# Performance work log

Measured on AMD Instinct MI355X. Metric: run time of the kernel, lower is better.

Reference implementation:

```python
import jax, jax.numpy as jnp
import numpy as np

B, S, DIM, HID, E, SE, K = 4, 2048, 1024, 1280, 8, 2, 2

def setup_inputs() -> dict:
    key = jax.random.key(0)
    ks = jax.random.split(key, 8)
    std = 0.02
    return {
        "x": jax.random.normal(ks[0], (B, S, DIM), jnp.float32),
        "expert_emb": jax.random.normal(ks[1], (E, DIM), jnp.float32),
        "gate_bias": jnp.zeros((E,), jnp.float32),
        "w1": jax.random.normal(ks[2], (E, HID, DIM), jnp.float32) * std,
        "w2": jax.random.normal(ks[3], (E, DIM, HID), jnp.float32) * std,
        "w3": jax.random.normal(ks[4], (E, HID, DIM), jnp.float32) * std,
        "sw1": jax.random.normal(ks[5], (SE, HID, DIM), jnp.float32) * std,
        "sw2": jax.random.normal(ks[6], (SE, DIM, HID), jnp.float32) * std,
        "sw3": jax.random.normal(ks[7], (SE, HID, DIM), jnp.float32) * std,
    }

def reference(x, expert_emb, gate_bias, w1, w2, w3, sw1, sw2, sw3):
    b, s, d = x.shape
    xt = x.reshape(-1, d)  # (T, D), T = B*S
    n_shared = sw1.shape[0]
    n_exp = w1.shape[0]
    k = K
    # shared experts: SwiGLU FFN, averaged over shared experts
    hs = jax.nn.silu(jnp.einsum('td,ehd->eth', xt, sw1)) * jnp.einsum('td,ehd->eth', xt, sw3)
    shared = jnp.einsum('eth,edh->td', hs, sw2) / n_shared  # mean over shared experts
    # gate: sigmoid scores + bias, top-k, normalized weights
    scores = jax.nn.sigmoid(xt @ expert_emb.T) + gate_bias  # (T, E)
    top_vals, top_idx = jax.lax.top_k(scores, k)            # (T, K)
    w = top_vals / jnp.sum(top_vals, axis=-1, keepdims=True)
    # per-token combine weight for each expert (0 if not routed)
    combine = jnp.sum((top_idx[..., None] == jnp.arange(n_exp)) * w[..., None], axis=1)  # (T, E)
    # routed experts: dense per-expert FFN, combined with routing weights
    hr = jax.nn.silu(jnp.einsum('td,ehd->eth', xt, w1)) * jnp.einsum('td,ehd->eth', xt, w3)
    out_e = jnp.einsum('eth,edh->etd', hr, w2)
    routed = jnp.einsum('etd,te->td', out_e, combine)
    out = (shared + routed).reshape(b, s, d)
    aux_loss = jnp.float32(0.0)  # eval mode: aux loss not computed
    routing_entropy = -jnp.sum(w * jnp.log(w), axis=-1).mean()
    return (out, aux_loss, routing_entropy)
```

## Files before the change

kernel.cpp:

```cpp
#include <hip/hip_runtime.h>
#include <math.h>

#define TOK 8192
#define DIMN 1024
#define HID 1280
#define NEXP 8
#define NSH 2
#define NSLOT 10
#define RCAP 17408
#define RCAPG (RCAP + 256)
#define G1_NT (DIMN / 64)
#define NGATE (TOK / 4)

typedef short s16x8 __attribute__((ext_vector_type(8)));
typedef float f32x4 __attribute__((ext_vector_type(4)));

__device__ __forceinline__ unsigned short f2bf(float f) {
  unsigned u = __float_as_uint(f);
  u += 0x7fffu + ((u >> 16) & 1u);
  return (unsigned short)(u >> 16);
}
__device__ __forceinline__ float bf2f(unsigned short u) {
  return __uint_as_float((unsigned)u << 16);
}

__device__ __forceinline__ void gl_lds16(const void* g, void* l) {
  typedef __attribute__((address_space(1))) const unsigned int guint;
  typedef __attribute__((address_space(3))) unsigned int luint;
  __builtin_amdgcn_global_load_lds((guint*)g, (luint*)l, 16, 0, 0);
}

__global__ __launch_bounds__(256) void k_zero(int* __restrict__ glist,
                                              int* __restrict__ cnt, int* __restrict__ cnt2) {
  int i = blockIdx.x * 256 + threadIdx.x;
  if (i < RCAPG) glist[i] = 0;
  if (i < NEXP) { cnt[i] = 0; cnt2[i] = 0; }
}

__global__ __launch_bounds__(256) void k_cvt_x(const float* __restrict__ x,
                                               unsigned short* __restrict__ xb) {
  int i = blockIdx.x * 256 + threadIdx.x;
  float4 v = ((const float4*)x)[i];
  ushort4 o;
  o.x = f2bf(v.x); o.y = f2bf(v.y); o.z = f2bf(v.z); o.w = f2bf(v.w);
  ((ushort4*)xb)[i] = o;
}

__global__ __launch_bounds__(256) void k_cvt_w(const float* __restrict__ w1, const float* __restrict__ w3,
                                               const float* __restrict__ sw1, const float* __restrict__ sw3,
                                               const float* __restrict__ w2, const float* __restrict__ sw2,
                                               unsigned short* __restrict__ w13b,
                                               unsigned short* __restrict__ w2b) {
  const int r = blockIdx.x;
  const int s = blockIdx.y;
  if (r < 2560) {
    const int which = (r >> 4) & 1;
    const int srow = ((r >> 5) << 4) + (r & 15);
    const float* src;
    if (s < NSH) src = (which ? sw3 : sw1) + ((size_t)s * HID + srow) * DIMN;
    else         src = (which ? w3 : w1) + ((size_t)(s - NSH) * HID + srow) * DIMN;
    unsigned short* dst = w13b + ((size_t)s * 2560 + r) * DIMN;
    int c = threadIdx.x * 4;
    float4 v = *(const float4*)(src + c);
    ushort4 o;
    o.x = f2bf(v.x); o.y = f2bf(v.y); o.z = f2bf(v.z); o.w = f2bf(v.w);
    *(ushort4*)(dst + c) = o;
  } else {
    const int d = r - 2560;
    const float* src = (s < NSH) ? sw2 + ((size_t)s * DIMN + d) * HID
                                 : w2 + ((size_t)(s - NSH) * DIMN + d) * HID;
    unsigned short* dst = w2b + ((size_t)s * DIMN + d) * HID;
    for (int c = threadIdx.x * 4; c < HID; c += 1024) {
      float4 v = *(const float4*)(src + c);
      ushort4 o;
      o.x = f2bf(v.x); o.y = f2bf(v.y); o.z = f2bf(v.z); o.w = f2bf(v.w);
      *(ushort4*)(dst + c) = o;
    }
  }
}

__global__ __launch_bounds__(256) void k_gate(const float* __restrict__ x, const float* __restrict__ emb,
                                              const float* __restrict__ bias, int* __restrict__ tidx,
                                              float* __restrict__ tw, float* __restrict__ entp) {
  const int lane = threadIdx.x & 63;
  const int wv = threadIdx.x >> 6;
  const int t = blockIdx.x * 4 + wv;
  const float* xr = x + (size_t)t * DIMN;
  float acc[NEXP];
#pragma unroll
  for (int e = 0; e < NEXP; ++e) acc[e] = 0.0f;
  for (int i = 0; i < DIMN / 64; ++i) {
    float xv = xr[lane + 64 * i];
#pragma unroll
    for (int e = 0; e < NEXP; ++e)
      acc[e] = fmaf(xv, emb[e * DIMN + lane + 64 * i], acc[e]);
  }
#pragma unroll
  for (int e = 0; e < NEXP; ++e) {
#pragma unroll
    for (int off = 32; off > 0; off >>= 1) acc[e] += __shfl_xor(acc[e], off);
  }
  __shared__ float ebuf[4];
  if (lane == 0) {
    float s[NEXP];
#pragma unroll
    for (int e = 0; e < NEXP; ++e) s[e] = 1.0f / (1.0f + expf(-acc[e])) + bias[e];
    int i0 = 0;
    for (int e = 1; e < NEXP; ++e) if (s[e] > s[i0]) i0 = e;
    int i1 = -1;
    for (int e = 0; e < NEXP; ++e) {
      if (e == i0) continue;
      if (i1 < 0 || s[e] > s[i1]) i1 = e;
    }
    float v0 = s[i0], v1 = s[i1];
    float inv = 1.0f / (v0 + v1);
    float w0 = v0 * inv, w1 = v1 * inv;
    tidx[2 * t] = i0; tidx[2 * t + 1] = i1;
    tw[2 * t] = w0; tw[2 * t + 1] = w1;
    ebuf[wv] = -(w0 * logf(w0) + w1 * logf(w1));
  }
  __syncthreads();
  if (threadIdx.x == 0) entp[blockIdx.x] = ebuf[0] + ebuf[1] + ebuf[2] + ebuf[3];
}

__global__ __launch_bounds__(256) void k_count(const int* __restrict__ tidx, int* __restrict__ cnt) {
  __shared__ int hist[NEXP];
  const int tid = threadIdx.x;
  if (tid < NEXP) hist[tid] = 0;
  __syncthreads();
  const int t = blockIdx.x * 256 + tid;
  atomicAdd(&hist[tidx[2 * t]], 1);
  atomicAdd(&hist[tidx[2 * t + 1]], 1);
  __syncthreads();
  if (tid < NEXP) atomicAdd(&cnt[tid], hist[tid]);
}

__global__ __launch_bounds__(256) void k_offsets(const int* __restrict__ cnt, int* __restrict__ roff,
                                                 int* __restrict__ cpad, const float* __restrict__ entp,
                                                 float* __restrict__ out_tail) {
  __shared__ float red[256];
  float s = 0.f;
  for (int i = threadIdx.x; i < NGATE; i += 256) s += entp[i];
  red[threadIdx.x] = s;
  __syncthreads();
  for (int st = 128; st > 0; st >>= 1) {
    if (threadIdx.x < st) red[threadIdx.x] += red[threadIdx.x + st];
    __syncthreads();
  }
  if (threadIdx.x == 0) {
    int off = 0;
    for (int e = 0; e < NEXP; ++e) {
      roff[e] = off;
      int cp = (cnt[e] + 127) & ~127;
      cpad[e] = cp;
      off += cp;
    }
    out_tail[0] = 0.f;
    out_tail[1] = red[0] / (float)TOK;
  }
}

__global__ __launch_bounds__(256) void k_scatter(const int* __restrict__ tidx,
                                                 const int* __restrict__ roff, int* __restrict__ cnt2,
                                                 int* __restrict__ glist, int* __restrict__ pos) {
  __shared__ int hist[NEXP], base[NEXP], cur[NEXP];
  const int tid = threadIdx.x;
  if (tid < NEXP) { hist[tid] = 0; cur[tid] = 0; }
  __syncthreads();
  const int t = blockIdx.x * 256 + tid;
  const int e0 = tidx[2 * t], e1 = tidx[2 * t + 1];
  atomicAdd(&hist[e0], 1);
  atomicAdd(&hist[e1], 1);
  __syncthreads();
  if (tid < NEXP) base[tid] = atomicAdd(&cnt2[tid], hist[tid]);
  __syncthreads();
  int p0 = atomicAdd(&cur[e0], 1);
  int g0 = roff[e0] + base[e0] + p0;
  glist[g0] = t; pos[2 * t] = g0;
  int p1 = atomicAdd(&cur[e1], 1);
  int g1 = roff[e1] + base[e1] + p1;
  glist[g1] = t; pos[2 * t + 1] = g1;
}

__global__ __launch_bounds__(512, 2) void k_gemm1_8ph(const unsigned short* __restrict__ xb,
                                                      const unsigned short* __restrict__ w13b,
                                                      unsigned short* __restrict__ h,
                                                      const int* __restrict__ glist,
                                                      const int* __restrict__ roff,
                                                      const int* __restrict__ cpad) {
  extern __shared__ __align__(16) char smem[];
  const int slot = blockIdx.z, yb = blockIdx.y, bx = blockIdx.x;
  const int tid = threadIdx.x;
  const int w = tid >> 6, lane = tid & 63;
  int hrow0, rowlim;
  int tokq[4];
  const int trbase = w * 8 + (lane >> 3);
  if (slot < NSH) {
    hrow0 = slot * TOK + yb * 256;
    rowlim = 256;
#pragma unroll
    for (int q = 0; q < 4; ++q) tokq[q] = yb * 256 + q * 64 + trbase;
  } else {
    const int e = slot - NSH;
    const int cp = cpad[e];
    if (yb * 256 >= cp) return;
    const int base = roff[e];
    hrow0 = 2 * TOK + base + yb * 256;
    rowlim = cp - yb * 256; if (rowlim > 256) rowlim = 256;
#pragma unroll
    for (int q = 0; q < 4; ++q) tokq[q] = glist[base + yb * 256 + q * 64 + trbase];
  }
  const int srcoff = ((lane & 7) * 16) ^ (((lane >> 4) & 1) << 4) ^ (((lane >> 5) & 1) << 5) ^ ((w & 1) << 6);
  const char* aptr[4];
#pragma unroll
  for (int q = 0; q < 4; ++q) aptr[q] = (const char*)xb + (size_t)tokq[q] * 2048 + srcoff;
  const char* w13s = (const char*)w13b + (size_t)slot * 2560 * 2048;
  const int crow0 = (w >> 2) * 64 + (w & 3) * 8 + (lane >> 3);
  const char* bptr[2];
#pragma unroll
  for (int nq = 0; nq < 2; ++nq)
    bptr[nq] = w13s + (size_t)(bx * 256 + crow0 + nq * 32) * 2048 + srcoff;
  const int dA = (w * 8) * 128;
  const int dB = 32768 + (((w >> 2) * 64 + (w & 3) * 8) * 128);

#define STA(BB, MH, TT) do {                               \
    char* _d = smem + (BB) + dA + (MH) * 8192;             \
    gl_lds16(aptr[MH] + (TT) * 128, _d);                   \
    gl_lds16(aptr[(MH) + 2] + (TT) * 128, _d + 16384);     \
  } while (0)
#define STB(BB, NQ, TT) do {                               \
    char* _d = smem + (BB) + dB + (NQ) * 4096;             \
    gl_lds16(bptr[NQ] + (TT) * 128, _d);                   \
    gl_lds16(bptr[NQ] + 262144 + (TT) * 128, _d + 16384);  \
  } while (0)

  const int lr = lane & 15, lq = lane >> 4;
  const int kswz = (((lr >> 1) & 1) << 4) | (((lr >> 2) & 1) << 5) | (((lr >> 3) & 1) << 6);
  const int wm = w >> 2, wn = w & 3;
  const int aoffb = (wm * 128 + lr) * 128 + lq * 16;
  const int boffb = 32768 + (wn * 64 + lr) * 128 + lq * 16;

#define RD_A(BB, MH) do {                                                                            \
    _Pragma("unroll")                                                                                \
    for (int mf = 0; mf < 4; ++mf)                                                                   \
      _Pragma("unroll")                                                                              \
      for (int ks = 0; ks < 2; ++ks)                                                                 \
        areg[mf][ks] = *(const s16x8*)(smem + (((BB) + aoffb + (MH) * 8192 + mf * 2048 + ks * 64) ^ kswz)); \
  } while (0)
#define RD_B(BB, NQ, RG) do {                                                                        \
    _Pragma("unroll")                                                                                \
    for (int nf = 0; nf < 2; ++nf)                                                                   \
      _Pragma("unroll")                                                                              \
      for (int ks = 0; ks < 2; ++ks)                                                                 \
        RG[nf][ks] = *(const s16x8*)(smem + (((BB) + boffb + (NQ) * 4096 + nf * 2048 + ks * 64) ^ kswz)); \
  } while (0)
#define MFMA16(MH, RG, NQ) do {                                                                      \
    __builtin_amdgcn_s_setprio(1);                                                                   \
    _Pragma("unroll")                                                                                \
    for (int mf = 0; mf < 4; ++mf)                                                                   \
      _Pragma("unroll")                                                                              \
      for (int nf = 0; nf < 2; ++nf)                                                                 \
        _Pragma("unroll")                                                                            \
        for (int ks = 0; ks < 2; ++ks)                                                               \
          acc[(MH) * 4 + mf][(NQ) * 2 + nf] = __builtin_amdgcn_mfma_f32_16x16x32_bf16(               \
              areg[mf][ks], RG[nf][ks], acc[(MH) * 4 + mf][(NQ) * 2 + nf], 0, 0, 0);                 \
    __builtin_amdgcn_s_setprio(0);                                                                   \
  } while (0)
#define VMW(N) asm volatile("s_waitcnt vmcnt(" #N ")" ::: "memory")
#define BARR() __builtin_amdgcn_s_barrier()
#define LGKM0() asm volatile("s_waitcnt lgkmcnt(0)" ::: "memory")

  STA(0, 0, 0); STB(0, 0, 0); STA(0, 1, 0); STB(0, 1, 0);
  STA(65536, 0, 1); STB(65536, 0, 1);
  VMW(8);
  BARR();

  f32x4 acc[8][4] = {};
  for (int j = 0; j < G1_NT; ++j) {
    const int bufb = (j & 1) << 16;
    const int bufo = bufb ^ 65536;
    const int t1 = (j + 1 < G1_NT) ? j + 1 : G1_NT - 1;
    const int t2 = (j + 2 < G1_NT) ? j + 2 : G1_NT - 1;
    s16x8 areg[4][2];
    s16x8 breg0[2][2], breg1[2][2];
    RD_A(bufb, 0);
    RD_B(bufb, 0, breg0);
    STA(bufo, 1, t1);
    VMW(6);
    BARR(); LGKM0();
    MFMA16(0, breg0, 0);
    BARR();
    RD_B(bufb, 1, breg1);
    STB(bufo, 1, t1);
    BARR(); LGKM0();
    MFMA16(0, breg1, 1);
    BARR();
    RD_A(bufb, 1);
    STA(bufb, 0, t2);
    BARR(); LGKM0();
    MFMA16(1, breg1, 1);
    BARR();
    STB(bufb, 0, t2);
    VMW(8);
    BARR();
    MFMA16(1, breg0, 0);
    BARR();
  }
#undef STA
#undef STB

  asm volatile("s_waitcnt vmcnt(0)" ::: "memory");
#pragma unroll
  for (int m = 0; m < 8; ++m) {
    const int lrow0 = wm * 128 + (m >> 2) * 64 + (m & 3) * 16 + lq * 4;
#pragma unroll
    for (int p = 0; p < 2; ++p) {
      f32x4 a1 = acc[m][2 * p];
      f32x4 a3 = acc[m][2 * p + 1];
      const int hc = (bx * 8 + wn * 2 + p) * 16 + lr;
#pragma unroll
      for (int r = 0; r < 4; ++r) {
        const int lrow = lrow0 + r;
        if (lrow < rowlim) {
          float u = a1[r];
          float hv = (u / (1.f + __expf(-u))) * a3[r];
          h[(size_t)(hrow0 + lrow) * HID + hc] = f2bf(hv);
        }
      }
    }
  }
#undef RD_A
#undef RD_B
#undef MFMA16
#undef VMW
#undef BARR
#undef LGKM0
}

__global__ __launch_bounds__(512, 2) void k_gemm2g(const unsigned short* __restrict__ h,
                                                   const unsigned short* __restrict__ w2b,
                                                   const int* __restrict__ roff,
                                                   const int* __restrict__ cpad,
                                                   float* __restrict__ out,
                                                   unsigned short* __restrict__ ro) {
  extern __shared__ __align__(16) char smem[];
  const int grp = blockIdx.z, bx = blockIdx.x, yb = blockIdx.y;
  const int tid = threadIdx.x;
  const int w = tid >> 6, lane = tid & 63;
  const int trbase = w * 8 + (lane >> 3);
  int nt, rowlim, base = 0;
  size_t arow0, arow1;
  if (grp == 0) {
    if (yb * 256 >= TOK) return;
    nt = 40; rowlim = 256;
    arow0 = (size_t)(yb * 256);
    arow1 = (size_t)(TOK + yb * 256);
  } else {
    const int e = grp - 1;
    const int cp = cpad[e];
    if (yb * 256 >= cp) return;
    base = roff[e];
    nt = 20;
    rowlim = cp - yb * 256; if (rowlim > 256) rowlim = 256;
    arow0 = (size_t)(2 * TOK + base + yb * 256);
    arow1 = arow0;
  }
  const int srcoff = ((lane & 7) * 16) ^ (((lane >> 4) & 1) << 4) ^ (((lane >> 5) & 1) << 5) ^ ((w & 1) << 6);
  const char* aptr0[4];
  const char* aptr1[4];
#pragma unroll
  for (int q = 0; q < 4; ++q) {
    int rq = q * 64 + trbase;
    if (grp != 0 && rq >= rowlim) rq = 0;
    aptr0[q] = (const char*)h + (arow0 + rq) * 2560 + srcoff;
    aptr1[q] = (const char*)h + (arow1 + rq) * 2560 + srcoff;
  }
  const int crow0 = (w >> 2) * 64 + (w & 3) * 8 + (lane >> 3);
  const char* bptr0[2];
  const char* bptr1[2];
#pragma unroll
  for (int nq = 0; nq < 2; ++nq) {
    const int bn = bx * 256 + crow0 + nq * 32;
    if (grp == 0) {
      bptr0[nq] = (const char*)w2b + (size_t)bn * 2560 + srcoff;
      bptr1[nq] = (const char*)w2b + (size_t)(1024 + bn) * 2560 + srcoff;
    } else {
      bptr0[nq] = (const char*)w2b + (size_t)((NSH + grp - 1) * 1024 + bn) * 2560 + srcoff;
      bptr1[nq] = bptr0[nq];
    }
  }
  const int dA = (w * 8) * 128;
  const int dB = 32768 + (((w >> 2) * 64 + (w & 3) * 8) * 128);

#define ASRC(Q, TT) ((TT) < 20 ? aptr0[Q] + (TT) * 128 : aptr1[Q] + ((TT) - 20) * 128)
#define BSRC(NQ, TT) ((TT) < 20 ? bptr0[NQ] + (TT) * 128 : bptr1[NQ] + ((TT) - 20) * 128)
#define STA(BB, MH, TT) do {                               \
    char* _d = smem + (BB) + dA + (MH) * 8192;             \
    gl_lds16(ASRC(MH, TT), _d);                            \
    gl_lds16(ASRC((MH) + 2, TT), _d + 16384);              \
  } while (0)
#define STB(BB, NQ, TT) do {                               \
    char* _d = smem + (BB) + dB + (NQ) * 4096;             \
    gl_lds16(BSRC(NQ, TT), _d);                            \
    gl_lds16(BSRC(NQ, TT) + (size_t)128 * 2560, _d + 16384); \
  } while (0)

  const int lr = lane & 15, lq = lane >> 4;
  const int kswz = (((lr >> 1) & 1) << 4) | (((lr >> 2) & 1) << 5) | (((lr >> 3) & 1) << 6);
  const int wm = w >> 2, wn = w & 3;
  const int aoffb = (wm * 128 + lr) * 128 + lq * 16;
  const int boffb = 32768 + (wn * 64 + lr) * 128 + lq * 16;

#define RD_A(BB, MH) do {                                                                            \
    _Pragma("unroll")                                                                                \
    for (int mf = 0; mf < 4; ++mf)                                                                   \
      _Pragma("unroll")                                                                              \
      for (int ks = 0; ks < 2; ++ks)                                                                 \
        areg[mf][ks] = *(const s16x8*)(smem + (((BB) + aoffb + (MH) * 8192 + mf * 2048 + ks * 64) ^ kswz)); \
  } while (0)
#define RD_B(BB, NQ, RG) do {                                                                        \
    _Pragma("unroll")                                                                                \
    for (int nf = 0; nf < 2; ++nf)                                                                   \
      _Pragma("unroll")                                                                              \
      for (int ks = 0; ks < 2; ++ks)                                                                 \
        RG[nf][ks] = *(const s16x8*)(smem + (((BB) + boffb + (NQ) * 4096 + nf * 2048 + ks * 64) ^ kswz)); \
  } while (0)
#define MFMA16(MH, RG, NQ) do {                                                                      \
    __builtin_amdgcn_s_setprio(1);                                                                   \
    _Pragma("unroll")                                                                                \
    for (int mf = 0; mf < 4; ++mf)                                                                   \
      _Pragma("unroll")                                                                              \
      for (int nf = 0; nf < 2; ++nf)                                                                 \
        _Pragma("unroll")                                                                            \
        for (int ks = 0; ks < 2; ++ks)                                                               \
          acc[(MH) * 4 + mf][(NQ) * 2 + nf] = __builtin_amdgcn_mfma_f32_16x16x32_bf16(               \
              areg[mf][ks], RG[nf][ks], acc[(MH) * 4 + mf][(NQ) * 2 + nf], 0, 0, 0);                 \
    __builtin_amdgcn_s_setprio(0);                                                                   \
  } while (0)
#define VMW(N) asm volatile("s_waitcnt vmcnt(" #N ")" ::: "memory")
#define BARR() __builtin_amdgcn_s_barrier()
#define LGKM0() asm volatile("s_waitcnt lgkmcnt(0)" ::: "memory")

  STA(0, 0, 0); STB(0, 0, 0); STA(0, 1, 0); STB(0, 1, 0);
  STA(65536, 0, 1); STB(65536, 0, 1);
  VMW(8);
  BARR();

  f32x4 acc[8][4] = {};
  for (int j = 0; j < nt; ++j) {
    const int bufb = (j & 1) << 16;
    const int bufo = bufb ^ 65536;
    const int t1 = (j + 1 < nt) ? j + 1 : nt - 1;
    const int t2 = (j + 2 < nt) ? j + 2 : nt - 1;
    s16x8 areg[4][2];
    s16x8 breg0[2][2], breg1[2][2];
    RD_A(bufb, 0);
    RD_B(bufb, 0, breg0);
    STA(bufo, 1, t1);
    VMW(6);
    BARR(); LGKM0();
    MFMA16(0, breg0, 0);
    BARR();
    RD_B(bufb, 1, breg1);
    STB(bufo, 1, t1);
    BARR(); LGKM0();
    MFMA16(0, breg1, 1);
    BARR();
    RD_A(bufb, 1);
    STA(bufb, 0, t2);
    BARR(); LGKM0();
    MFMA16(1, breg1, 1);
    BARR();
    STB(bufb, 0, t2);
    VMW(8);
    BARR();
    MFMA16(1, breg0, 0);
    BARR();
  }
#undef STA
#undef STB
#undef ASRC
#undef BSRC

  asm volatile("s_waitcnt vmcnt(0)" ::: "memory");
  if (grp == 0) {
#pragma unroll
    for (int m = 0; m < 8; ++m) {
      const int lrow0 = wm * 128 + (m >> 2) * 64 + (m & 3) * 16 + lq * 4;
#pragma unroll
      for (int nf = 0; nf < 4; ++nf) {
        const int col = bx * 256 + wn * 64 + nf * 16 + lr;
#pragma unroll
        for (int r = 0; r < 4; ++r)
          out[(size_t)(yb * 256 + lrow0 + r) * DIMN + col] = 0.5f * acc[m][nf][r];
      }
    }
  } else {
#pragma unroll
    for (int m = 0; m < 8; ++m) {
      const int lrow0 = wm * 128 + (m >> 2) * 64 + (m & 3) * 16 + lq * 4;
#pragma unroll
      for (int r = 0; r < 4; ++r) {
        const int lrow = lrow0 + r;
        if (lrow < rowlim) {
          const size_t g = (size_t)(base + yb * 256 + lrow);
#pragma unroll
          for (int nf = 0; nf < 4; ++nf) {
            const int col = bx * 256 + wn * 64 + nf * 16 + lr;
            ro[g * DIMN + col] = f2bf(acc[m][nf][r]);
          }
        }
      }
    }
  }
#undef RD_A
#undef RD_B
#undef MFMA16
#undef VMW
#undef BARR
#undef LGKM0
}

__global__ __launch_bounds__(256) void k_combine(const unsigned short* __restrict__ ro,
                                                 const int* __restrict__ pos,
                                                 const float* __restrict__ tw,
                                                 float* __restrict__ out) {
  const int t = blockIdx.x;
  const int g0 = pos[2 * t], g1 = pos[2 * t + 1];
  const float w0 = tw[2 * t], w1 = tw[2 * t + 1];
  const int c = threadIdx.x * 4;
  ushort4 r0 = *(const ushort4*)(ro + (size_t)g0 * DIMN + c);
  ushort4 r1 = *(const ushort4*)(ro + (size_t)g1 * DIMN + c);
  float4 o = *(float4*)(out + (size_t)t * DIMN + c);
  o.x += w0 * bf2f(r0.x) + w1 * bf2f(r1.x);
  o.y += w0 * bf2f(r0.y) + w1 * bf2f(r1.y);
  o.z += w0 * bf2f(r0.z) + w1 * bf2f(r1.z);
  o.w += w0 * bf2f(r0.w) + w1 * bf2f(r1.w);
  *(float4*)(out + (size_t)t * DIMN + c) = o;
}

static const size_t OFF_XB    = 0;
static const size_t OFF_W13   = OFF_XB + (size_t)TOK * DIMN * 2;
static const size_t OFF_W2    = OFF_W13 + (size_t)NSLOT * 2560 * DIMN * 2;
static const size_t OFF_H     = OFF_W2 + (size_t)NSLOT * DIMN * HID * 2;
static const size_t OFF_RO    = OFF_W13;
static const size_t OFF_GLIST = OFF_H + (size_t)(2 * TOK + RCAP) * HID * 2;
static const size_t OFF_POS   = OFF_GLIST + (size_t)RCAPG * 4;
static const size_t OFF_TIDX  = OFF_POS + (size_t)TOK * 2 * 4;
static const size_t OFF_TW    = OFF_TIDX + (size_t)TOK * 2 * 4;
static const size_t OFF_ENTP  = OFF_TW + (size_t)TOK * 2 * 4;
static const size_t OFF_CNT   = OFF_ENTP + (size_t)NGATE * 4;
static const size_t OFF_CNT2  = OFF_CNT + 32;
static const size_t OFF_ROFF  = OFF_CNT2 + 32;
static const size_t OFF_CPAD  = OFF_ROFF + 32;

extern "C" void kernel_launch(void* const* d_in, const int* in_sizes, int n_in,
                              void* d_out, int out_size, void* d_ws, size_t ws_size,
                              hipStream_t stream) {
  const float* x    = (const float*)d_in[0];
  const float* emb  = (const float*)d_in[1];
  const float* bias = (const float*)d_in[2];
  const float* w1   = (const float*)d_in[3];
  const float* w2   = (const float*)d_in[4];
  const float* w3   = (const float*)d_in[5];
  const float* sw1  = (const float*)d_in[6];
  const float* sw2  = (const float*)d_in[7];
  const float* sw3  = (const float*)d_in[8];
  float* out = (float*)d_out;
  char* ws = (char*)d_ws;
  unsigned short* xb   = (unsigned short*)(ws + OFF_XB);
  unsigned short* w13b = (unsigned short*)(ws + OFF_W13);
  unsigned short* w2b  = (unsigned short*)(ws + OFF_W2);
  unsigned short* h    = (unsigned short*)(ws + OFF_H);
  unsigned short* ro   = (unsigned short*)(ws + OFF_RO);
  int*   glist = (int*)(ws + OFF_GLIST);
  int*   pos   = (int*)(ws + OFF_POS);
  int*   tidx  = (int*)(ws + OFF_TIDX);
  float* tw    = (float*)(ws + OFF_TW);
  float* entp  = (float*)(ws + OFF_ENTP);
  int*   cnt   = (int*)(ws + OFF_CNT);
  int*   cnt2  = (int*)(ws + OFF_CNT2);
  int*   roff  = (int*)(ws + OFF_ROFF);
  int*   cpad  = (int*)(ws + OFF_CPAD);

  hipFuncSetAttribute((const void*)k_gemm1_8ph, hipFuncAttributeMaxDynamicSharedMemorySize, 131072);
  hipFuncSetAttribute((const void*)k_gemm2g, hipFuncAttributeMaxDynamicSharedMemorySize, 131072);

  k_zero<<<(RCAPG + 255) / 256, 256, 0, stream>>>(glist, cnt, cnt2);
  k_cvt_x<<<(TOK * DIMN / 4) / 256, 256, 0, stream>>>(x, xb);
  k_cvt_w<<<dim3(2560 + DIMN, NSLOT), 256, 0, stream>>>(w1, w3, sw1, sw3, w2, sw2, w13b, w2b);
  k_gate<<<NGATE, 256, 0, stream>>>(x, emb, bias, tidx, tw, entp);
  k_count<<<TOK / 256, 256, 0, stream>>>(tidx, cnt);
  k_offsets<<<1, 256, 0, stream>>>(cnt, roff, cpad, entp, out + (size_t)TOK * DIMN);
  k_scatter<<<TOK / 256, 256, 0, stream>>>(tidx, roff, cnt2, glist, pos);
  k_gemm1_8ph<<<dim3(10, TOK / 256, NSLOT), 512, 131072, stream>>>(xb, w13b, h, glist, roff, cpad);
  k_gemm2g<<<dim3(DIMN / 256, TOK / 256, 1 + NEXP), 512, 131072, stream>>>(h, w2b, roff, cpad, out, ro);
  k_combine<<<TOK, 256, 0, stream>>>(ro, pos, tw, out);
}
```

Measured before the change: 427.2 us.

## Fuse x bf16 conversion into gate and software-pipeline gemm1 LDS reads with MFMA

Removes the separate x-to-bf16 conversion kernel and writes the bf16 copy inside the gate kernel, which already reads x, saving one full pass over the activations and one launch. In gemm1, LDS fragment loads are double-buffered into separate A register sets and issued ahead of the MFMAs that use them. The explicit lgkmcnt waits are replaced by scheduling barriers so that LDS reads overlap with matrix math. The extra register arrays raise register pressure in a kernel launched with a 512-thread, two-blocks-per-unit bound. The gate kernel now does narrow 2-byte strided stores, which may coalesce poorly.

```diff
diff --git a/kernel.cpp b/kernel.cpp
--- a/kernel.cpp
+++ b/kernel.cpp
@@ -35,15 +35,6 @@
   int i = blockIdx.x * 256 + threadIdx.x;
   if (i < RCAPG) glist[i] = 0;
   if (i < NEXP) { cnt[i] = 0; cnt2[i] = 0; }
-}
-
-__global__ __launch_bounds__(256) void k_cvt_x(const float* __restrict__ x,
-                                               unsigned short* __restrict__ xb) {
-  int i = blockIdx.x * 256 + threadIdx.x;
-  float4 v = ((const float4*)x)[i];
-  ushort4 o;
-  o.x = f2bf(v.x); o.y = f2bf(v.y); o.z = f2bf(v.z); o.w = f2bf(v.w);
-  ((ushort4*)xb)[i] = o;
 }
 
 __global__ __launch_bounds__(256) void k_cvt_w(const float* __restrict__ w1, const float* __restrict__ w3,
@@ -80,17 +71,21 @@
 }
 
 __global__ __launch_bounds__(256) void k_gate(const float* __restrict__ x, const float* __restrict__ emb,
-                                              const float* __restrict__ bias, int* __restrict__ tidx,
+                                              const float* __restrict__ bias,
+                                              unsigned short* __restrict__ xb,
+                                              int* __restrict__ tidx,
                                               float* __restrict__ tw, float* __restrict__ entp) {
   const int lane = threadIdx.x & 63;
   const int wv = threadIdx.x >> 6;
   const int t = blockIdx.x * 4 + wv;
   const float* xr = x + (size_t)t * DIMN;
+  unsigned short* xbr = xb + (size_t)t * DIMN;
   float acc[NEXP];
 #pragma unroll
   for (int e = 0; e < NEXP; ++e) acc[e] = 0.0f;
   for (int i = 0; i < DIMN / 64; ++i) {
     float xv = xr[lane + 64 * i];
+    xbr[lane + 64 * i] = f2bf(xv);
 #pragma unroll
     for (int e = 0; e < NEXP; ++e)
       acc[e] = fmaf(xv, emb[e * DIMN + lane + 64 * i], acc[e]);
@@ -240,12 +235,12 @@
   const int aoffb = (wm * 128 + lr) * 128 + lq * 16;
   const int boffb = 32768 + (wn * 64 + lr) * 128 + lq * 16;
 
-#define RD_A(BB, MH) do {                                                                            \
+#define RD_A(BB, MH, AR) do {                                                                        \
     _Pragma("unroll")                                                                                \
     for (int mf = 0; mf < 4; ++mf)                                                                   \
       _Pragma("unroll")                                                                              \
       for (int ks = 0; ks < 2; ++ks)                                                                 \
-        areg[mf][ks] = *(const s16x8*)(smem + (((BB) + aoffb + (MH) * 8192 + mf * 2048 + ks * 64) ^ kswz)); \
+        AR[mf][ks] = *(const s16x8*)(smem + (((BB) + aoffb + (MH) * 8192 + mf * 2048 + ks * 64) ^ kswz)); \
   } while (0)
 #define RD_B(BB, NQ, RG) do {                                                                        \
     _Pragma("unroll")                                                                                \
@@ -254,7 +249,7 @@
       for (int ks = 0; ks < 2; ++ks)                                                                 \
         RG[nf][ks] = *(const s16x8*)(smem + (((BB) + boffb + (NQ) * 4096 + nf * 2048 + ks * 64) ^ kswz)); \
   } while (0)
-#define MFMA16(MH, RG, NQ) do {                                                                      \
+#define MFMA16(AR, RG, MH, NQ) do {                                                                  \
     __builtin_amdgcn_s_setprio(1);                                                                   \
     _Pragma("unroll")                                                                                \
     for (int mf = 0; mf < 4; ++mf)                                                                   \
@@ -263,17 +258,21 @@
         _Pragma("unroll")                                                                            \
         for (int ks = 0; ks < 2; ++ks)                                                               \
           acc[(MH) * 4 + mf][(NQ) * 2 + nf] = __builtin_amdgcn_mfma_f32_16x16x32_bf16(               \
-              areg[mf][ks], RG[nf][ks], acc[(MH) * 4 + mf][(NQ) * 2 + nf], 0, 0, 0);                 \
+              AR[mf][ks], RG[nf][ks], acc[(MH) * 4 + mf][(NQ) * 2 + nf], 0, 0, 0);                   \
     __builtin_amdgcn_s_setprio(0);                                                                   \
   } while (0)
 #define VMW(N) asm volatile("s_waitcnt vmcnt(" #N ")" ::: "memory")
 #define BARR() __builtin_amdgcn_s_barrier()
-#define LGKM0() asm volatile("s_waitcnt lgkmcnt(0)" ::: "memory")
+#define SCHEDB() __builtin_amdgcn_sched_barrier(0)
 
   STA(0, 0, 0); STB(0, 0, 0); STA(0, 1, 0); STB(0, 1, 0);
   STA(65536, 0, 1); STB(65536, 0, 1);
   VMW(8);
-  BARR();
+  BARR(); SCHEDB();
+  s16x8 aregA[4][2], aregB[4][2];
+  s16x8 breg0[2][2], breg1[2][2];
+  RD_A(0, 0, aregA);
+  RD_B(0, 0, breg0);
 
   f32x4 acc[8][4] = {};
   for (int j = 0; j < G1_NT; ++j) {
@@ -281,29 +280,27 @@
     const int bufo = bufb ^ 65536;
     const int t1 = (j + 1 < G1_NT) ? j + 1 : G1_NT - 1;
     const int t2 = (j + 2 < G1_NT) ? j + 2 : G1_NT - 1;
-    s16x8 areg[4][2];
-    s16x8 breg0[2][2], breg1[2][2];
-    RD_A(bufb, 0);
-    RD_B(bufb, 0, breg0);
     STA(bufo, 1, t1);
     VMW(6);
-    BARR(); LGKM0();
-    MFMA16(0, breg0, 0);
-    BARR();
+    BARR(); SCHEDB();
     RD_B(bufb, 1, breg1);
+    MFMA16(aregA, breg0, 0, 0);
+    BARR();
     STB(bufo, 1, t1);
-    BARR(); LGKM0();
-    MFMA16(0, breg1, 1);
-    BARR();
-    RD_A(bufb, 1);
+    BARR();
+    RD_A(bufb, 1, aregB);
+    MFMA16(aregA, breg1, 0, 1);
+    BARR();
     STA(bufb, 0, t2);
-    BARR(); LGKM0();
-    MFMA16(1, breg1, 1);
+    BARR();
+    MFMA16(aregB, breg1, 1, 1);
     BARR();
     STB(bufb, 0, t2);
     VMW(8);
-    BARR();
-    MFMA16(1, breg0, 0);
+    BARR(); SCHEDB();
+    MFMA16(aregB, breg0, 1, 0);
+    RD_A(bufo, 0, aregA);
+    RD_B(bufo, 0, breg0);
     BARR();
   }
 #undef STA
@@ -334,7 +331,7 @@
 #undef MFMA16
 #undef VMW
 #undef BARR
-#undef LGKM0
+#undef SCHEDB
 }
 
 __global__ __launch_bounds__(512, 2) void k_gemm2g(const unsigned short* __restrict__ h,
@@ -587,9 +584,8 @@
   hipFuncSetAttribute((const void*)k_gemm2g, hipFuncAttributeMaxDynamicSharedMemorySize, 131072);
 
   k_zero<<<(RCAPG + 255) / 256, 256, 0, stream>>>(glist, cnt, cnt2);
-  k_cvt_x<<<(TOK * DIMN / 4) / 256, 256, 0, stream>>>(x, xb);
   k_cvt_w<<<dim3(2560 + DIMN, NSLOT), 256, 0, stream>>>(w1, w3, sw1, sw3, w2, sw2, w13b, w2b);
-  k_gate<<<NGATE, 256, 0, stream>>>(x, emb, bias, tidx, tw, entp);
+  k_gate<<<NGATE, 256, 0, stream>>>(x, emb, bias, xb, tidx, tw, entp);
   k_count<<<TOK / 256, 256, 0, stream>>>(tidx, cnt);
   k_offsets<<<1, 256, 0, stream>>>(cnt, roff, cpad, entp, out + (size_t)TOK * DIMN);
   k_scatter<<<TOK / 256, 256, 0, stream>>>(tidx, roff, cnt2, glist, pos);
```

Result: no change. 435.5 us (+1.9%).
